# Kernel optimization log

Hardware: AMD Instinct MI355X
Metric: run time of the kernel (lower is better)

The kernel has to match this reference:

```python
import jax, jax.numpy as jnp
import numpy as np

N_NODES = 200000
EMBED_DIM = 64
N_EDGES = 5000000


def setup_inputs() -> dict:
    key = jax.random.key(0)
    k1, k2 = jax.random.split(key)
    x = jax.random.normal(k1, (N_NODES, EMBED_DIM), dtype=jnp.float32)
    edge_index = jax.random.randint(k2, (2, N_EDGES), 0, N_NODES, dtype=jnp.int64)
    return {"x": x, "edge_index": edge_index}


def _lightgcn_forward(x, edge_index):
    # x: [N, d], edge_index: [2, E]
    n = x.shape[0]
    loop = jnp.arange(n, dtype=edge_index.dtype)
    row = jnp.concatenate([edge_index[0], loop])  # add_self_loop
    col = jnp.concatenate([edge_index[1], loop])
    w = jnp.ones(row.shape[0], dtype=x.dtype)

    # deg = unsorted_segment_sum(edge_weight, row); transition = diag(1/deg) @ adj
    deg = jax.ops.segment_sum(w, row, num_segments=n)
    inv_deg = 1.0 / (deg + 1e-8)
    w = w * inv_deg[row]

    # gcn_norm_adj(transition): symmetric D^{-1/2} A D^{-1/2} on transition weights
    deg2 = jax.ops.segment_sum(w, row, num_segments=n)
    inv_sqrt = jnp.where(deg2 > 0, jax.lax.rsqrt(deg2 + 1e-8), 0.0)
    w = inv_sqrt[row] * w * inv_sqrt[col]

    # h = normed_adj @ x  (SpMM: gather neighbor embeddings, scale, scatter-add)
    h = jax.ops.segment_sum(w[:, None] * x[col], row, num_segments=n)
    return h


def reference(x, edge_index):
    return _lightgcn_forward(x, edge_index)
```

## Files before the change

kernel.cpp:

```cpp
#include <hip/hip_runtime.h>


#define D 64
#define RSHIFT 8
#define RPB 256
#define CAP 8192
#define NBLK_SC 256

typedef unsigned short ushort_t;

__device__ __forceinline__ ushort_t f2bf(float f) {
    unsigned u = __float_as_uint(f);
    return (ushort_t)((u + 0x7FFFu + ((u >> 16) & 1u)) >> 16);
}

__global__ __launch_bounds__(256)
void scatter_kernel(const int* __restrict__ rows, const int* __restrict__ cols,
                    int* __restrict__ gcur, unsigned int* __restrict__ packed,
                    int E, int B) {
    __shared__ int cnt[1024];
    int blk = blockIdx.x;
    int per = (((E + NBLK_SC - 1) / NBLK_SC) + 3) & ~3;
    int lo = min(E, blk * per);
    int hi = min(E, lo + per);
    int m = hi - lo;

    for (int i = threadIdx.x; i < B; i += 256) cnt[i] = 0;
    __syncthreads();

    int nv = m >> 2;
    const int4* r4 = (const int4*)(rows + lo);
    for (int t = threadIdx.x; t < nv; t += 256) {
        int4 v = r4[t];
        atomicAdd(&cnt[v.x >> RSHIFT], 1);
        atomicAdd(&cnt[v.y >> RSHIFT], 1);
        atomicAdd(&cnt[v.z >> RSHIFT], 1);
        atomicAdd(&cnt[v.w >> RSHIFT], 1);
    }
    for (int k = (nv << 2) + threadIdx.x; k < m; k += 256)
        atomicAdd(&cnt[rows[lo + k] >> RSHIFT], 1);
    __syncthreads();

    for (int i = threadIdx.x; i < B; i += 256) {
        int c = cnt[i];
        cnt[i] = (c > 0) ? atomicAdd(&gcur[i], c) : 0;
    }
    __syncthreads();

    const int4* c4 = (const int4*)(cols + lo);
    for (int t = threadIdx.x; t < nv; t += 256) {
        int4 r = r4[t];
        int4 c = c4[t];
        int pos;
        pos = atomicAdd(&cnt[r.x >> RSHIFT], 1);
        if (pos < CAP) packed[(size_t)(r.x >> RSHIFT) * CAP + pos] =
            ((unsigned)(r.x & (RPB - 1)) << 18) | (unsigned)c.x;
        pos = atomicAdd(&cnt[r.y >> RSHIFT], 1);
        if (pos < CAP) packed[(size_t)(r.y >> RSHIFT) * CAP + pos] =
            ((unsigned)(r.y & (RPB - 1)) << 18) | (unsigned)c.y;
        pos = atomicAdd(&cnt[r.z >> RSHIFT], 1);
        if (pos < CAP) packed[(size_t)(r.z >> RSHIFT) * CAP + pos] =
            ((unsigned)(r.z & (RPB - 1)) << 18) | (unsigned)c.z;
        pos = atomicAdd(&cnt[r.w >> RSHIFT], 1);
        if (pos < CAP) packed[(size_t)(r.w >> RSHIFT) * CAP + pos] =
            ((unsigned)(r.w & (RPB - 1)) << 18) | (unsigned)c.w;
    }
    for (int k = (nv << 2) + threadIdx.x; k < m; k += 256) {
        int r = rows[lo + k];
        int c = cols[lo + k];
        int pos = atomicAdd(&cnt[r >> RSHIFT], 1);
        if (pos < CAP) packed[(size_t)(r >> RSHIFT) * CAP + pos] =
            ((unsigned)(r & (RPB - 1)) << 18) | (unsigned)c;
    }
}

__global__ __launch_bounds__(RPB)
void sort_kernel(unsigned int* __restrict__ packed, const int* __restrict__ gcur,
                 int* __restrict__ rs, int* __restrict__ re,
                 float* __restrict__ afac,
                 const float* __restrict__ x, ushort_t* __restrict__ y,
                 int B, int n) {
    __shared__ unsigned int buf[CAP];
    __shared__ int cnt[RPB];
    __shared__ int part[RPB];
    __shared__ int cur[RPB];
    __shared__ float bf[RPB];
    int bkt = blockIdx.x;
    int tid = threadIdx.x;
    int m = min(gcur[bkt], CAP);
    size_t base = (size_t)bkt * CAP;

    cnt[tid] = 0;
    __syncthreads();

    int nv = m >> 2;
    const uint4* p4 = (const uint4*)(packed + base);
    for (int t = tid; t < nv; t += RPB) {
        uint4 w = p4[t];
        int k = t << 2;
        buf[k + 0] = w.x;
        buf[k + 1] = w.y;
        buf[k + 2] = w.z;
        buf[k + 3] = w.w;
        atomicAdd(&cnt[w.x >> 18], 1);
        atomicAdd(&cnt[w.y >> 18], 1);
        atomicAdd(&cnt[w.z >> 18], 1);
        atomicAdd(&cnt[w.w >> 18], 1);
    }
    for (int k = (nv << 2) + tid; k < m; k += RPB) {
        unsigned w = packed[base + k];
        buf[k] = w;
        atomicAdd(&cnt[w >> 18], 1);
    }
    __syncthreads();

    int deg = cnt[tid];
    part[tid] = deg;
    __syncthreads();
    for (int off = 1; off < RPB; off <<= 1) {
        int t = (tid >= off) ? part[tid - off] : 0;
        __syncthreads();
        part[tid] += t;
        __syncthreads();
    }
    int excl = part[tid] - deg;
    cur[tid] = excl;

    float degf = (float)(deg + 1);
    float inv_deg = 1.0f / (degf + 1e-8f);
    float deg2 = degf * inv_deg;
    float inv_sqrt = rsqrtf(deg2 + 1e-8f);
    bf[tid] = inv_sqrt;
    int r0 = bkt << RSHIFT;
    int r = r0 + tid;
    if (r < n) {
        rs[r] = (int)(base + excl);
        re[r] = (int)(base + excl + deg);
        afac[r] = inv_sqrt * inv_deg;
    }
    __syncthreads();

    int nrow = min(RPB, n - r0);
    const float4* x4 = (const float4*)x;
    ushort4* y4 = (ushort4*)y;
    for (int idx = tid; idx < nrow * 16; idx += RPB) {
        int row = idx >> 4;
        int q = idx & 15;
        float b = bf[row];
        float4 v = x4[(size_t)(r0 + row) * 16 + q];
        ushort4 o;
        o.x = f2bf(b * v.x);
        o.y = f2bf(b * v.y);
        o.z = f2bf(b * v.z);
        o.w = f2bf(b * v.w);
        y4[(size_t)(r0 + row) * 16 + q] = o;
    }

    for (int k = tid; k < m; k += RPB) {
        unsigned w = buf[k];
        int pos = atomicAdd(&cur[w >> 18], 1);
        packed[base + pos] = w & 0x3FFFFu;
    }
}

__device__ __forceinline__ void acc_bf4(float4& a, uint2 u) {
    a.x += __uint_as_float(u.x << 16);
    a.y += __uint_as_float(u.x & 0xFFFF0000u);
    a.z += __uint_as_float(u.y << 16);
    a.w += __uint_as_float(u.y & 0xFFFF0000u);
}

__global__ __launch_bounds__(256)
void spmm_kernel(const int* __restrict__ rs, const int* __restrict__ re,
                 const unsigned int* __restrict__ cols,
                 const float* __restrict__ afac,
                 const uint2* __restrict__ y64,
                 float* __restrict__ h, int n) {
    int gid = blockIdx.x * blockDim.x + threadIdx.x;
    int r = gid >> 6;
    if (r >= n) return;
    int lane = gid & 63;
    int g = lane & 15;
    int p = lane >> 4;

    int s = rs[r];
    int e = re[r];

    float4 acc0 = {0.f, 0.f, 0.f, 0.f};
    float4 acc1 = acc0, acc2 = acc0, acc3 = acc0;
    if (p == 0) acc_bf4(acc0, y64[(size_t)r * 16 + g]);

    int k = s;
    for (; k + 16 <= e; k += 16) {
        int c0 = (int)cols[k + 0 + p];
        int c1 = (int)cols[k + 4 + p];
        int c2 = (int)cols[k + 8 + p];
        int c3 = (int)cols[k + 12 + p];
        uint2 u0 = y64[(size_t)c0 * 16 + g];
        uint2 u1 = y64[(size_t)c1 * 16 + g];
        uint2 u2 = y64[(size_t)c2 * 16 + g];
        uint2 u3 = y64[(size_t)c3 * 16 + g];
        acc_bf4(acc0, u0);
        acc_bf4(acc1, u1);
        acc_bf4(acc2, u2);
        acc_bf4(acc3, u3);
    }
    for (; k + 4 <= e; k += 4) {
        int c = (int)cols[k + p];
        acc_bf4(acc1, y64[(size_t)c * 16 + g]);
    }
    int rem = e - k;
    if (p < rem) {
        int c = (int)cols[k + p];
        acc_bf4(acc2, y64[(size_t)c * 16 + g]);
    }

    float4 t;
    t.x = (acc0.x + acc1.x) + (acc2.x + acc3.x);
    t.y = (acc0.y + acc1.y) + (acc2.y + acc3.y);
    t.z = (acc0.z + acc1.z) + (acc2.z + acc3.z);
    t.w = (acc0.w + acc1.w) + (acc2.w + acc3.w);
    t.x += __shfl_xor(t.x, 16, 64);  t.x += __shfl_xor(t.x, 32, 64);
    t.y += __shfl_xor(t.y, 16, 64);  t.y += __shfl_xor(t.y, 32, 64);
    t.z += __shfl_xor(t.z, 16, 64);  t.z += __shfl_xor(t.z, 32, 64);
    t.w += __shfl_xor(t.w, 16, 64);  t.w += __shfl_xor(t.w, 32, 64);

    if (p == 0) {
        float a = afac[r];
        float4 out = {a * t.x, a * t.y, a * t.z, a * t.w};
        *reinterpret_cast<float4*>(&h[(size_t)r * D + 4 * g]) = out;
    }
}

extern "C" void kernel_launch(void* const* d_in, const int* in_sizes, int n_in,
                              void* d_out, int out_size, void* d_ws, size_t ws_size,
                              hipStream_t stream) {
    const float* x = (const float*)d_in[0];
    const int* edge = (const int*)d_in[1];
    float* h = (float*)d_out;

    int n = in_sizes[0] / D;
    int E = in_sizes[1] / 2;
    const int* rows = edge;
    const int* cols = edge + E;

    int B = (n + RPB - 1) >> RSHIFT;

    char* p = (char*)d_ws;
    int* gcur       = (int*)p;        p += 800 * 4;
    int* rs         = (int*)p;        p += (size_t)n * 4;
    int* re         = (int*)p;        p += (size_t)n * 4;
    float* afac     = (float*)p;      p += (size_t)n * 4;
    unsigned int* packed = (unsigned int*)p;  p += (size_t)B * CAP * 4;
    ushort_t* y     = (ushort_t*)p;

    hipMemsetAsync(gcur, 0, (size_t)B * sizeof(int), stream);
    scatter_kernel<<<NBLK_SC, 256, 0, stream>>>(rows, cols, gcur, packed, E, B);
    sort_kernel<<<B, RPB, 0, stream>>>(packed, gcur, rs, re, afac, x, y, B, n);
    spmm_kernel<<<(n * 64 + 255) / 256, 256, 0, stream>>>(rs, re, packed, afac,
                                                          (const uint2*)y, h, n);
}
```

Baseline: 212.0 us.

## Widen SpMM gathers to 16-byte loads, use non-temporal access, double sort threads

```diff
diff --git a/kernel.cpp b/kernel.cpp
--- a/kernel.cpp
+++ b/kernel.cpp
@@ -6,8 +6,10 @@
 #define RPB 256
 #define CAP 8192
 #define NBLK_SC 256
+#define SORT_T 512
 
 typedef unsigned short ushort_t;
+typedef float vfloat4 __attribute__((ext_vector_type(4)));
 
 __device__ __forceinline__ ushort_t f2bf(float f) {
     unsigned u = __float_as_uint(f);
@@ -74,7 +76,7 @@
     }
 }
 
-__global__ __launch_bounds__(RPB)
+__global__ __launch_bounds__(SORT_T)
 void sort_kernel(unsigned int* __restrict__ packed, const int* __restrict__ gcur,
                  int* __restrict__ rs, int* __restrict__ re,
                  float* __restrict__ afac,
@@ -90,12 +92,12 @@
     int m = min(gcur[bkt], CAP);
     size_t base = (size_t)bkt * CAP;
 
-    cnt[tid] = 0;
+    if (tid < RPB) cnt[tid] = 0;
     __syncthreads();
 
     int nv = m >> 2;
     const uint4* p4 = (const uint4*)(packed + base);
-    for (int t = tid; t < nv; t += RPB) {
+    for (int t = tid; t < nv; t += SORT_T) {
         uint4 w = p4[t];
         int k = t << 2;
         buf[k + 0] = w.x;
@@ -107,43 +109,45 @@
         atomicAdd(&cnt[w.z >> 18], 1);
         atomicAdd(&cnt[w.w >> 18], 1);
     }
-    for (int k = (nv << 2) + tid; k < m; k += RPB) {
+    for (int k = (nv << 2) + tid; k < m; k += SORT_T) {
         unsigned w = packed[base + k];
         buf[k] = w;
         atomicAdd(&cnt[w >> 18], 1);
     }
     __syncthreads();
 
-    int deg = cnt[tid];
-    part[tid] = deg;
+    int deg = (tid < RPB) ? cnt[tid] : 0;
+    if (tid < RPB) part[tid] = deg;
     __syncthreads();
     for (int off = 1; off < RPB; off <<= 1) {
-        int t = (tid >= off) ? part[tid - off] : 0;
+        int t = (tid < RPB && tid >= off) ? part[tid - off] : 0;
         __syncthreads();
-        part[tid] += t;
+        if (tid < RPB) part[tid] += t;
         __syncthreads();
     }
-    int excl = part[tid] - deg;
-    cur[tid] = excl;
-
-    float degf = (float)(deg + 1);
-    float inv_deg = 1.0f / (degf + 1e-8f);
-    float deg2 = degf * inv_deg;
-    float inv_sqrt = rsqrtf(deg2 + 1e-8f);
-    bf[tid] = inv_sqrt;
+
     int r0 = bkt << RSHIFT;
-    int r = r0 + tid;
-    if (r < n) {
-        rs[r] = (int)(base + excl);
-        re[r] = (int)(base + excl + deg);
-        afac[r] = inv_sqrt * inv_deg;
+    if (tid < RPB) {
+        int excl = part[tid] - deg;
+        cur[tid] = excl;
+        float degf = (float)(deg + 1);
+        float inv_deg = 1.0f / (degf + 1e-8f);
+        float deg2 = degf * inv_deg;
+        float inv_sqrt = rsqrtf(deg2 + 1e-8f);
+        bf[tid] = inv_sqrt;
+        int r = r0 + tid;
+        if (r < n) {
+            rs[r] = (int)(base + excl);
+            re[r] = (int)(base + excl + deg);
+            afac[r] = inv_sqrt * inv_deg;
+        }
     }
     __syncthreads();
 
     int nrow = min(RPB, n - r0);
     const float4* x4 = (const float4*)x;
     ushort4* y4 = (ushort4*)y;
-    for (int idx = tid; idx < nrow * 16; idx += RPB) {
+    for (int idx = tid; idx < nrow * 16; idx += SORT_T) {
         int row = idx >> 4;
         int q = idx & 15;
         float b = bf[row];
@@ -156,79 +160,85 @@
         y4[(size_t)(r0 + row) * 16 + q] = o;
     }
 
-    for (int k = tid; k < m; k += RPB) {
+    for (int k = tid; k < m; k += SORT_T) {
         unsigned w = buf[k];
         int pos = atomicAdd(&cur[w >> 18], 1);
         packed[base + pos] = w & 0x3FFFFu;
     }
 }
 
-__device__ __forceinline__ void acc_bf4(float4& a, uint2 u) {
+__device__ __forceinline__ void acc_bf8(float4& a, float4& b, uint4 u) {
     a.x += __uint_as_float(u.x << 16);
     a.y += __uint_as_float(u.x & 0xFFFF0000u);
     a.z += __uint_as_float(u.y << 16);
     a.w += __uint_as_float(u.y & 0xFFFF0000u);
+    b.x += __uint_as_float(u.z << 16);
+    b.y += __uint_as_float(u.z & 0xFFFF0000u);
+    b.z += __uint_as_float(u.w << 16);
+    b.w += __uint_as_float(u.w & 0xFFFF0000u);
 }
 
 __global__ __launch_bounds__(256)
 void spmm_kernel(const int* __restrict__ rs, const int* __restrict__ re,
                  const unsigned int* __restrict__ cols,
                  const float* __restrict__ afac,
-                 const uint2* __restrict__ y64,
+                 const uint4* __restrict__ y128,
                  float* __restrict__ h, int n) {
     int gid = blockIdx.x * blockDim.x + threadIdx.x;
     int r = gid >> 6;
     if (r >= n) return;
     int lane = gid & 63;
-    int g = lane & 15;
-    int p = lane >> 4;
+    int g = lane & 7;
+    int p = lane >> 3;
 
     int s = rs[r];
     int e = re[r];
 
-    float4 acc0 = {0.f, 0.f, 0.f, 0.f};
-    float4 acc1 = acc0, acc2 = acc0, acc3 = acc0;
-    if (p == 0) acc_bf4(acc0, y64[(size_t)r * 16 + g]);
+    float4 a0 = {0.f, 0.f, 0.f, 0.f}, b0 = a0, a1 = a0, b1 = a0;
+    if (p == 0) acc_bf8(a0, b0, y128[(size_t)r * 8 + g]);
 
     int k = s;
     for (; k + 16 <= e; k += 16) {
-        int c0 = (int)cols[k + 0 + p];
-        int c1 = (int)cols[k + 4 + p];
-        int c2 = (int)cols[k + 8 + p];
-        int c3 = (int)cols[k + 12 + p];
-        uint2 u0 = y64[(size_t)c0 * 16 + g];
-        uint2 u1 = y64[(size_t)c1 * 16 + g];
-        uint2 u2 = y64[(size_t)c2 * 16 + g];
-        uint2 u3 = y64[(size_t)c3 * 16 + g];
-        acc_bf4(acc0, u0);
-        acc_bf4(acc1, u1);
-        acc_bf4(acc2, u2);
-        acc_bf4(acc3, u3);
-    }
-    for (; k + 4 <= e; k += 4) {
-        int c = (int)cols[k + p];
-        acc_bf4(acc1, y64[(size_t)c * 16 + g]);
+        int c0 = (int)__builtin_nontemporal_load(&cols[k + p]);
+        int c1 = (int)__builtin_nontemporal_load(&cols[k + 8 + p]);
+        uint4 u0 = y128[(size_t)c0 * 8 + g];
+        uint4 u1 = y128[(size_t)c1 * 8 + g];
+        acc_bf8(a0, b0, u0);
+        acc_bf8(a1, b1, u1);
+    }
+    if (k + 8 <= e) {
+        int c = (int)__builtin_nontemporal_load(&cols[k + p]);
+        acc_bf8(a0, b0, y128[(size_t)c * 8 + g]);
+        k += 8;
     }
     int rem = e - k;
     if (p < rem) {
-        int c = (int)cols[k + p];
-        acc_bf4(acc2, y64[(size_t)c * 16 + g]);
-    }
-
-    float4 t;
-    t.x = (acc0.x + acc1.x) + (acc2.x + acc3.x);
-    t.y = (acc0.y + acc1.y) + (acc2.y + acc3.y);
-    t.z = (acc0.z + acc1.z) + (acc2.z + acc3.z);
-    t.w = (acc0.w + acc1.w) + (acc2.w + acc3.w);
-    t.x += __shfl_xor(t.x, 16, 64);  t.x += __shfl_xor(t.x, 32, 64);
-    t.y += __shfl_xor(t.y, 16, 64);  t.y += __shfl_xor(t.y, 32, 64);
-    t.z += __shfl_xor(t.z, 16, 64);  t.z += __shfl_xor(t.z, 32, 64);
-    t.w += __shfl_xor(t.w, 16, 64);  t.w += __shfl_xor(t.w, 32, 64);
+        int c = (int)__builtin_nontemporal_load(&cols[k + p]);
+        acc_bf8(a1, b1, y128[(size_t)c * 8 + g]);
+    }
+
+    float4 ta, tb;
+    ta.x = a0.x + a1.x;  ta.y = a0.y + a1.y;  ta.z = a0.z + a1.z;  ta.w = a0.w + a1.w;
+    tb.x = b0.x + b1.x;  tb.y = b0.y + b1.y;  tb.z = b0.z + b1.z;  tb.w = b0.w + b1.w;
+    #pragma unroll
+    for (int off = 8; off <= 32; off <<= 1) {
+        ta.x += __shfl_xor(ta.x, off, 64);
+        ta.y += __shfl_xor(ta.y, off, 64);
+        ta.z += __shfl_xor(ta.z, off, 64);
+        ta.w += __shfl_xor(ta.w, off, 64);
+        tb.x += __shfl_xor(tb.x, off, 64);
+        tb.y += __shfl_xor(tb.y, off, 64);
+        tb.z += __shfl_xor(tb.z, off, 64);
+        tb.w += __shfl_xor(tb.w, off, 64);
+    }
 
     if (p == 0) {
         float a = afac[r];
-        float4 out = {a * t.x, a * t.y, a * t.z, a * t.w};
-        *reinterpret_cast<float4*>(&h[(size_t)r * D + 4 * g]) = out;
+        vfloat4 oa = {a * ta.x, a * ta.y, a * ta.z, a * ta.w};
+        vfloat4 ob = {a * tb.x, a * tb.y, a * tb.z, a * tb.w};
+        vfloat4* hp = reinterpret_cast<vfloat4*>(&h[(size_t)r * D + 8 * g]);
+        __builtin_nontemporal_store(oa, hp);
+        __builtin_nontemporal_store(ob, hp + 1);
     }
 }
 
@@ -256,7 +266,7 @@
 
     hipMemsetAsync(gcur, 0, (size_t)B * sizeof(int), stream);
     scatter_kernel<<<NBLK_SC, 256, 0, stream>>>(rows, cols, gcur, packed, E, B);
-    sort_kernel<<<B, RPB, 0, stream>>>(packed, gcur, rs, re, afac, x, y, B, n);
+    sort_kernel<<<B, SORT_T, 0, stream>>>(packed, gcur, rs, re, afac, x, y, B, n);
     spmm_kernel<<<(n * 64 + 255) / 256, 256, 0, stream>>>(rs, re, packed, afac,
-                                                          (const uint2*)y, h, n);
-}
+                                                          (const uint4*)y, h, n);
+}
```

Result: no change. 212.3 us (+0.2%).
